# Optimization experiments

Measured on AMD Instinct MI355X. Metric: run time of the kernel, lower is better.

The kernel has to match this reference:

```python
import jax, jax.numpy as jnp
import numpy as np

L, H, C, D = 4, 4, 64, 64  # layers, heads, per-head out channels, embedding_dim
NEG_SLOPE = 0.2
LN_EPS = 1e-5

def layer_norm(x, g, b):
    mu = x.mean(-1, keepdims=True)
    var = ((x - mu) ** 2).mean(-1, keepdims=True)
    return (x - mu) * jax.lax.rsqrt(var + LN_EPS) * g + b

def setup_inputs() -> dict:
    key = jax.random.key(0)
    N, E = 20000, 320000
    ks = jax.random.split(key, 12)
    f = lambda k, shape: jax.random.normal(k, shape, jnp.float32) * 0.1
    return {
        "node_feats": jax.random.normal(ks[0], (N, D), jnp.float32),
        "edge_feats": jax.random.normal(ks[1], (E, D), jnp.float32),
        "edge_index": jax.random.randint(ks[2], (2, E), 0, N),
        "W_lin": f(ks[3], (L, D, H * C)),      # GAT node projection (bias=False)
        "W_edge": f(ks[4], (L, D, H * C)),     # GAT edge projection (bias=False)
        "att_src": f(ks[5], (L, H, C)),
        "att_dst": f(ks[6], (L, H, C)),
        "att_edge": f(ks[7], (L, H, C)),
        "bias_conv": f(ks[8], (L, D)),
        "ln_g": jnp.ones((L, D), jnp.float32),
        "ln_b": jnp.zeros((L, D), jnp.float32),
        "eW1": f(ks[9], (L, 3 * D, 3 * D)),
        "eb1": jnp.zeros((L, 3 * D), jnp.float32),
        "eln_g": jnp.ones((L, 3 * D), jnp.float32),
        "eln_b": jnp.zeros((L, 3 * D), jnp.float32),
        "eW2": f(ks[10], (L, 3 * D, D)),
        "eb2": jnp.zeros((L, D), jnp.float32),
    }

def reference(node_feats, edge_feats, edge_index, W_lin, W_edge, att_src,
              att_dst, att_edge, bias_conv, ln_g, ln_b, eW1, eb1, eln_g,
              eln_b, eW2, eb2):
    N = node_feats.shape[0]
    src, dst = edge_index[0], edge_index[1]
    for l in range(L):
        # --- GAT attention conv (concat=False: mean over heads) ---
        x = (node_feats @ W_lin[l]).reshape(N, H, C)
        e = (edge_feats @ W_edge[l]).reshape(-1, H, C)
        x_j, x_i = x[src], x[dst]                                  # [E,H,C]
        alpha = ((x_j * att_src[l]).sum(-1) + (x_i * att_dst[l]).sum(-1)
                 + (e * att_edge[l]).sum(-1))                      # [E,H]
        alpha = jax.nn.leaky_relu(alpha, NEG_SLOPE)
        amax = jax.ops.segment_max(alpha, dst, num_segments=N)
        alpha = jnp.exp(alpha - amax[dst])
        denom = jax.ops.segment_sum(alpha, dst, num_segments=N)
        alpha = alpha / (denom[dst] + 1e-16)
        out = jax.ops.segment_sum(x_j * alpha[..., None], dst, num_segments=N)
        out = out.mean(axis=1) + bias_conv[l]                      # [N,D]
        node_feats = layer_norm(out, ln_g[l], ln_b[l])
        # --- SparseEdgeUpdateLayer (residual=True) ---
        ni, nj = node_feats[src], node_feats[dst]
        h = jnp.concatenate([ni + nj, jnp.abs(ni - nj), edge_feats], axis=-1)
        h = jax.nn.relu(layer_norm(h @ eW1[l] + eb1[l], eln_g[l], eln_b[l]))
        edge_feats = h @ eW2[l] + eb2[l] + edge_feats
        # dropout is identity in eval mode
        if l < L - 1:
            node_feats = jax.nn.relu(node_feats)
    return node_feats, edge_feats
```

## Files before the change

kernel.cpp:

```cpp
#include <hip/hip_runtime.h>
#include <math.h>

#define NLAYERS 4
#define H 4
#define C 64
#define D 64
#define HC 256
#define D3 192
#define NEG 0.2f

typedef float f32x4 __attribute__((ext_vector_type(4)));
typedef short bf16x8 __attribute__((ext_vector_type(8)));
typedef unsigned short u16;

__device__ __forceinline__ u16 f2bf(float f) {
    unsigned u = __float_as_uint(f);
    u += 0x7FFFu + ((u >> 16) & 1u);
    return (u16)(u >> 16);
}
__device__ __forceinline__ float bf2f(u16 h) {
    return __uint_as_float((unsigned)h << 16);
}

__global__ void k_weffs(const float* __restrict__ W_edge, const float* __restrict__ att_edge,
                        const float* __restrict__ W_lin, const float* __restrict__ att_s,
                        const float* __restrict__ att_d,
                        float* __restrict__ weff, float* __restrict__ w_asd) {
    int l = blockIdx.x;
    const float* We = W_edge + (size_t)l * D * HC;
    const float* Wl = W_lin + (size_t)l * D * HC;
    const float* ae = att_edge + l * H * C;
    const float* as_ = att_s + l * H * C;
    const float* ad = att_d + l * H * C;
    int t = threadIdx.x;
    int d = t >> 2, h = t & 3;
    float se = 0.f, ss = 0.f, sd = 0.f;
    #pragma unroll
    for (int c = 0; c < C; ++c) {
        float we = We[d * HC + h * C + c];
        float wl = Wl[d * HC + h * C + c];
        se = fmaf(we, ae[h * C + c], se);
        ss = fmaf(wl, as_[h * C + c], ss);
        sd = fmaf(wl, ad[h * C + c], sd);
    }
    weff[l * HC + d * 4 + h] = se;
    w_asd[l * 512 + d * 8 + h] = ss;
    w_asd[l * 512 + d * 8 + 4 + h] = sd;
}

__global__ void k_cvtw(const float* __restrict__ W1, const float* __restrict__ W2,
                       u16* __restrict__ W1T, u16* __restrict__ W2T) {
    int i = blockIdx.x * 256 + threadIdx.x;
    if (i < NLAYERS * D3 * D3) {
        int l = i / (D3 * D3), r = i % (D3 * D3);
        int n = r / D3, k = r % D3;
        W1T[i] = f2bf(W1[l * D3 * D3 + k * D3 + n]);
    } else {
        int j = i - NLAYERS * D3 * D3;
        if (j < NLAYERS * D3 * D) {
            int l = j / (D3 * D), r = j % (D3 * D);
            int n = r / D3, k = r % D3;
            W2T[j] = f2bf(W2[l * D3 * D + k * D + n]);
        }
    }
}

__global__ void k_cvtwl(const float* __restrict__ W_lin,
                        u16* __restrict__ WTh, u16* __restrict__ WTl) {
    int i = blockIdx.x * 256 + threadIdx.x;
    if (i >= NLAYERS * HC * D) return;
    int l = i / (HC * D), r = i % (HC * D);
    int o = r / D, d = r % D;
    float v = W_lin[(size_t)l * D * HC + d * HC + o];
    u16 h = f2bf(v);
    WTh[i] = h;
    WTl[i] = f2bf(v - bf2f(h));
}

__global__ void k_hist(const int* __restrict__ dst, int* __restrict__ deg, int E) {
    int i = blockIdx.x * blockDim.x + threadIdx.x;
    if (i < E) atomicAdd(&deg[dst[i]], 1);
}

__global__ void k_scan(const int* __restrict__ deg, int* __restrict__ rowptr,
                       int* __restrict__ head, int N, int E) {
    __shared__ int lds[1024];
    int t = threadIdx.x;
    int chunk = (N + 1023) / 1024;
    int begin = t * chunk, end = min(begin + chunk, N);
    int sum = 0;
    for (int i = begin; i < end; ++i) sum += deg[i];
    lds[t] = sum;
    __syncthreads();
    for (int off = 1; off < 1024; off <<= 1) {
        int v = (t >= off) ? lds[t - off] : 0;
        __syncthreads();
        lds[t] += v;
        __syncthreads();
    }
    int running = (t == 0) ? 0 : lds[t - 1];
    for (int i = begin; i < end; ++i) {
        int dg = deg[i];
        rowptr[i] = running;
        head[i] = running;
        running += dg;
    }
    if (t == 0) rowptr[N] = E;
}

__global__ void k_scatter(const int* __restrict__ src, const int* __restrict__ dst,
                          int* __restrict__ head, int* __restrict__ csrpos,
                          int* __restrict__ perm_src, int E) {
    int i = blockIdx.x * blockDim.x + threadIdx.x;
    if (i < E) {
        int d = dst[i];
        int pos = atomicAdd(&head[d], 1);
        csrpos[i] = pos;
        perm_src[pos] = src[i];
    }
}

__global__ __launch_bounds__(256, 4) void k_nodeproj_mfma(
    const float* __restrict__ nf, const u16* __restrict__ WTh, const u16* __restrict__ WTl,
    const float* __restrict__ w_asd, float* __restrict__ x,
    float* __restrict__ a_src, float* __restrict__ a_dst, int N, int relu_in) {
    __shared__ __align__(16) u16 s_ah[32 * 72];
    __shared__ __align__(16) u16 s_al[32 * 72];
    __shared__ __align__(16) float s_nf[32][68];
    __shared__ __align__(16) float s_wasd[512];
    int tid = threadIdx.x;
    int w = tid >> 6, lane = tid & 63;
    int n0 = blockIdx.x << 5;

    if (tid < 128) *(float4*)&s_wasd[tid * 4] = *(const float4*)&w_asd[tid * 4];

    {
        int r = tid >> 3, c0 = (tid & 7) << 3;
        int n = n0 + r;
        float4 v0 = make_float4(0.f, 0.f, 0.f, 0.f), v1 = v0;
        if (n < N) {
            v0 = *(const float4*)&nf[(size_t)n * D + c0];
            v1 = *(const float4*)&nf[(size_t)n * D + c0 + 4];
        }
        if (relu_in) {
            v0.x = fmaxf(v0.x, 0.f); v0.y = fmaxf(v0.y, 0.f);
            v0.z = fmaxf(v0.z, 0.f); v0.w = fmaxf(v0.w, 0.f);
            v1.x = fmaxf(v1.x, 0.f); v1.y = fmaxf(v1.y, 0.f);
            v1.z = fmaxf(v1.z, 0.f); v1.w = fmaxf(v1.w, 0.f);
        }
        *(float4*)&s_nf[r][c0] = v0;
        *(float4*)&s_nf[r][c0 + 4] = v1;
        float vv[8] = {v0.x, v0.y, v0.z, v0.w, v1.x, v1.y, v1.z, v1.w};
        bf16x8 hv, lv;
        #pragma unroll
        for (int j = 0; j < 8; ++j) {
            u16 h = f2bf(vv[j]);
            hv[j] = (short)h;
            lv[j] = (short)f2bf(vv[j] - bf2f(h));
        }
        *(bf16x8*)&s_ah[r * 72 + c0] = hv;
        *(bf16x8*)&s_al[r * 72 + c0] = lv;
    }
    __syncthreads();

    int m16 = lane & 15, quad = lane >> 4, kq = quad * 8;
    f32x4 acc[2][4];
    #pragma unroll
    for (int mt = 0; mt < 2; ++mt)
        #pragma unroll
        for (int nt = 0; nt < 4; ++nt) {
            acc[mt][nt][0] = 0.f; acc[mt][nt][1] = 0.f;
            acc[mt][nt][2] = 0.f; acc[mt][nt][3] = 0.f;
        }
    #pragma unroll
    for (int ks = 0; ks < 2; ++ks) {
        int ko = ks * 32 + kq;
        bf16x8 ah0 = *(const bf16x8*)&s_ah[m16 * 72 + ko];
        bf16x8 ah1 = *(const bf16x8*)&s_ah[(16 + m16) * 72 + ko];
        bf16x8 al0 = *(const bf16x8*)&s_al[m16 * 72 + ko];
        bf16x8 al1 = *(const bf16x8*)&s_al[(16 + m16) * 72 + ko];
        #pragma unroll
        for (int nt = 0; nt < 4; ++nt) {
            int col = w * 64 + nt * 16 + m16;
            bf16x8 bh = *(const bf16x8*)&WTh[col * D + ko];
            bf16x8 bl = *(const bf16x8*)&WTl[col * D + ko];
            acc[0][nt] = __builtin_amdgcn_mfma_f32_16x16x32_bf16(ah0, bh, acc[0][nt], 0, 0, 0);
            acc[0][nt] = __builtin_amdgcn_mfma_f32_16x16x32_bf16(al0, bh, acc[0][nt], 0, 0, 0);
            acc[0][nt] = __builtin_amdgcn_mfma_f32_16x16x32_bf16(ah0, bl, acc[0][nt], 0, 0, 0);
            acc[1][nt] = __builtin_amdgcn_mfma_f32_16x16x32_bf16(ah1, bh, acc[1][nt], 0, 0, 0);
            acc[1][nt] = __builtin_amdgcn_mfma_f32_16x16x32_bf16(al1, bh, acc[1][nt], 0, 0, 0);
            acc[1][nt] = __builtin_amdgcn_mfma_f32_16x16x32_bf16(ah1, bl, acc[1][nt], 0, 0, 0);
        }
    }
    #pragma unroll
    for (int mt = 0; mt < 2; ++mt) {
        #pragma unroll
        for (int nt = 0; nt < 4; ++nt) {
            int col = w * 64 + nt * 16 + m16;
            #pragma unroll
            for (int r = 0; r < 4; ++r) {
                int n = n0 + mt * 16 + quad * 4 + r;
                if (n < N) x[(size_t)n * HC + col] = acc[mt][nt][r];
            }
        }
    }

    {
        int nloc = tid >> 3, o = tid & 7;
        float s = 0.f;
        #pragma unroll
        for (int d = 0; d < 64; ++d)
            s = fmaf(s_nf[nloc][d], s_wasd[d * 8 + o], s);
        int n = n0 + nloc;
        if (n < N) {
            if (o < 4) a_src[n * 4 + o] = s;
            else       a_dst[n * 4 + (o - 4)] = s;
        }
    }
}

__global__ void k_alpha(const float* __restrict__ ef, const float* __restrict__ weff,
                        const int* __restrict__ src, const int* __restrict__ dst,
                        const float* __restrict__ a_src, const float* __restrict__ a_dst,
                        const int* __restrict__ csrpos, float* __restrict__ alpha_csr, int E) {
    int wave = (int)((blockIdx.x * blockDim.x + threadIdx.x) >> 6);
    int lane = threadIdx.x & 63;
    int sub = lane >> 4, li = lane & 15;
    int e = wave * 4 + sub;
    if (e >= E) return;
    float4 efv = *(const float4*)&ef[(size_t)e * D + li * 4];
    float4 w0 = *(const float4*)&weff[(li * 4 + 0) * 4];
    float4 w1 = *(const float4*)&weff[(li * 4 + 1) * 4];
    float4 w2 = *(const float4*)&weff[(li * 4 + 2) * 4];
    float4 w3 = *(const float4*)&weff[(li * 4 + 3) * 4];
    float p0 = efv.x * w0.x + efv.y * w1.x + efv.z * w2.x + efv.w * w3.x;
    float p1 = efv.x * w0.y + efv.y * w1.y + efv.z * w2.y + efv.w * w3.y;
    float p2 = efv.x * w0.z + efv.y * w1.z + efv.z * w2.z + efv.w * w3.z;
    float p3 = efv.x * w0.w + efv.y * w1.w + efv.z * w2.w + efv.w * w3.w;
    #pragma unroll
    for (int off = 1; off < 16; off <<= 1) {
        p0 += __shfl_xor(p0, off);
        p1 += __shfl_xor(p1, off);
        p2 += __shfl_xor(p2, off);
        p3 += __shfl_xor(p3, off);
    }
    if (li < 4) {
        float p = (li == 0) ? p0 : (li == 1) ? p1 : (li == 2) ? p2 : p3;
        int s = src[e], dd = dst[e];
        float a = p + a_src[s * 4 + li] + a_dst[dd * 4 + li];
        a = (a > 0.f) ? a : NEG * a;
        alpha_csr[(size_t)csrpos[e] * 4 + li] = a;
    }
}

__global__ void k_alpha_lite(const float* __restrict__ palpha,
                             const int* __restrict__ src, const int* __restrict__ dst,
                             const float* __restrict__ a_src, const float* __restrict__ a_dst,
                             const int* __restrict__ csrpos, float* __restrict__ alpha_csr, int E) {
    int i = blockIdx.x * 256 + threadIdx.x;
    if (i >= E * 4) return;
    int e = i >> 2, h = i & 3;
    float a = palpha[i] + a_src[src[e] * 4 + h] + a_dst[dst[e] * 4 + h];
    a = (a > 0.f) ? a : NEG * a;
    alpha_csr[(size_t)csrpos[e] * 4 + h] = a;
}

__global__ void k_gat(const float* __restrict__ x, float* __restrict__ alpha_csr,
                      const int* __restrict__ rowptr, const int* __restrict__ perm_src,
                      const float* __restrict__ bias, const float* __restrict__ g,
                      const float* __restrict__ b, float* __restrict__ nf_ln,
                      float* __restrict__ out2, int N) {
    int n = (int)((blockIdx.x * blockDim.x + threadIdx.x) >> 6);
    int lane = threadIdx.x & 63;
    if (n >= N) return;
    int s = rowptr[n], e = rowptr[n + 1];
    int deg = e - s;
    float m0 = -1e30f, m1 = -1e30f, m2 = -1e30f, m3 = -1e30f;
    for (int i = lane; i < deg; i += 64) {
        const float4 a = *(const float4*)&alpha_csr[(size_t)(s + i) * 4];
        m0 = fmaxf(m0, a.x); m1 = fmaxf(m1, a.y);
        m2 = fmaxf(m2, a.z); m3 = fmaxf(m3, a.w);
    }
    #pragma unroll
    for (int off = 32; off; off >>= 1) {
        m0 = fmaxf(m0, __shfl_xor(m0, off)); m1 = fmaxf(m1, __shfl_xor(m1, off));
        m2 = fmaxf(m2, __shfl_xor(m2, off)); m3 = fmaxf(m3, __shfl_xor(m3, off));
    }
    float d0 = 0.f, d1 = 0.f, d2 = 0.f, d3 = 0.f;
    for (int i = lane; i < deg; i += 64) {
        float4 a = *(const float4*)&alpha_csr[(size_t)(s + i) * 4];
        a.x = expf(a.x - m0); a.y = expf(a.y - m1);
        a.z = expf(a.z - m2); a.w = expf(a.w - m3);
        *(float4*)&alpha_csr[(size_t)(s + i) * 4] = a;
        d0 += a.x; d1 += a.y; d2 += a.z; d3 += a.w;
    }
    #pragma unroll
    for (int off = 32; off; off >>= 1) {
        d0 += __shfl_xor(d0, off); d1 += __shfl_xor(d1, off);
        d2 += __shfl_xor(d2, off); d3 += __shfl_xor(d3, off);
    }
    float i0 = 0.25f / (d0 + 1e-16f), i1 = 0.25f / (d1 + 1e-16f);
    float i2 = 0.25f / (d2 + 1e-16f), i3 = 0.25f / (d3 + 1e-16f);
    float ac0 = 0.f, ac1 = 0.f, ac2 = 0.f, ac3 = 0.f;
    int j = 0;
    for (; j + 3 < deg; j += 4) {
        const float4 a0 = *(const float4*)&alpha_csr[(size_t)(s + j + 0) * 4];
        const float4 a1 = *(const float4*)&alpha_csr[(size_t)(s + j + 1) * 4];
        const float4 a2 = *(const float4*)&alpha_csr[(size_t)(s + j + 2) * 4];
        const float4 a3 = *(const float4*)&alpha_csr[(size_t)(s + j + 3) * 4];
        int s0 = perm_src[s + j + 0], s1 = perm_src[s + j + 1];
        int s2 = perm_src[s + j + 2], s3 = perm_src[s + j + 3];
        const float* x0 = x + (size_t)s0 * HC;
        const float* x1 = x + (size_t)s1 * HC;
        const float* x2 = x + (size_t)s2 * HC;
        const float* x3 = x + (size_t)s3 * HC;
        ac0 += a0.x * i0 * x0[lane] + a0.y * i1 * x0[64 + lane]
             + a0.z * i2 * x0[128 + lane] + a0.w * i3 * x0[192 + lane];
        ac1 += a1.x * i0 * x1[lane] + a1.y * i1 * x1[64 + lane]
             + a1.z * i2 * x1[128 + lane] + a1.w * i3 * x1[192 + lane];
        ac2 += a2.x * i0 * x2[lane] + a2.y * i1 * x2[64 + lane]
             + a2.z * i2 * x2[128 + lane] + a2.w * i3 * x2[192 + lane];
        ac3 += a3.x * i0 * x3[lane] + a3.y * i1 * x3[64 + lane]
             + a3.z * i2 * x3[128 + lane] + a3.w * i3 * x3[192 + lane];
    }
    for (; j < deg; ++j) {
        const float4 a = *(const float4*)&alpha_csr[(size_t)(s + j) * 4];
        int sidx = perm_src[s + j];
        const float* xr = x + (size_t)sidx * HC;
        ac0 += a.x * i0 * xr[lane] + a.y * i1 * xr[64 + lane]
             + a.z * i2 * xr[128 + lane] + a.w * i3 * xr[192 + lane];
    }
    float acc = (ac0 + ac1) + (ac2 + ac3);
    float v = acc + bias[lane];
    float sm = v;
    #pragma unroll
    for (int off = 32; off; off >>= 1) sm += __shfl_xor(sm, off);
    float mu = sm * (1.f / 64.f);
    float dv = v - mu;
    float q = dv * dv;
    #pragma unroll
    for (int off = 32; off; off >>= 1) q += __shfl_xor(q, off);
    float rstd = rsqrtf(q * (1.f / 64.f) + 1e-5f);
    float r = dv * rstd * g[lane] + b[lane];
    nf_ln[(size_t)n * D + lane] = r;
    if (out2) out2[(size_t)n * D + lane] = r;
}

__global__ __launch_bounds__(256, 5) void k_edgemlp_mfma(
    const float* __restrict__ nf, const float* __restrict__ ef_in,
    const int* __restrict__ src, const int* __restrict__ dst,
    const u16* __restrict__ W1T, const float* __restrict__ b1,
    const float* __restrict__ lg, const float* __restrict__ lb,
    const u16* __restrict__ W2T, const float* __restrict__ b2,
    float* __restrict__ ef_out, const float* __restrict__ weffN,
    float* __restrict__ palpha, int E) {
    __shared__ __align__(16) u16 A1[64 * 200];
    __shared__ float ps[4][64], pq[4][64];
    int tid = threadIdx.x;
    int w = tid >> 6, lane = tid & 63;
    int e0 = blockIdx.x * 64;
    int ebase = e0 + w * 16;

    int idxv = 0;
    if (lane < 16)      idxv = src[min(ebase + lane, E - 1)];
    else if (lane < 32) idxv = dst[min(ebase + lane - 16, E - 1)];

    {
        int half = lane >> 5;
        int c2 = (lane & 31) << 1;
        #pragma unroll
        for (int it = 0; it < 8; ++it) {
            int eloc = 2 * it + half;
            int ge = ebase + eloc;
            int sA = __shfl(idxv, eloc);
            int dA = __shfl(idxv, 16 + eloc);
            float2 za = make_float2(0.f, 0.f), zb = za, zf = za;
            if (ge < E) {
                za = *(const float2*)&nf[(size_t)sA * D + c2];
                zb = *(const float2*)&nf[(size_t)dA * D + c2];
                zf = *(const float2*)&ef_in[(size_t)ge * D + c2];
            }
            unsigned su = (unsigned)f2bf(za.x + zb.x) | ((unsigned)f2bf(za.y + zb.y) << 16);
            unsigned du = (unsigned)f2bf(fabsf(za.x - zb.x)) | ((unsigned)f2bf(fabsf(za.y - zb.y)) << 16);
            unsigned fu = (unsigned)f2bf(zf.x) | ((unsigned)f2bf(zf.y) << 16);
            int row = w * 16 + eloc;
            *(unsigned*)&A1[row * 200 + c2]       = su;
            *(unsigned*)&A1[row * 200 + 64 + c2]  = du;
            *(unsigned*)&A1[row * 200 + 128 + c2] = fu;
        }
    }
    __syncthreads();

    int m16 = lane & 15, quad = lane >> 4, kq = quad * 8;
    f32x4 acc[4][3];
    #pragma unroll
    for (int nt = 0; nt < 3; ++nt) {
        float bv = b1[w * 48 + nt * 16 + m16];
        #pragma unroll
        for (int mt = 0; mt < 4; ++mt) {
            acc[mt][nt][0] = bv; acc[mt][nt][1] = bv;
            acc[mt][nt][2] = bv; acc[mt][nt][3] = bv;
        }
    }
    #pragma unroll
    for (int ks = 0; ks < 6; ++ks) {
        int ko = ks * 32 + kq;
        bf16x8 af0 = *(const bf16x8*)&A1[(0  + m16) * 200 + ko];
        bf16x8 af1 = *(const bf16x8*)&A1[(16 + m16) * 200 + ko];
        bf16x8 af2 = *(const bf16x8*)&A1[(32 + m16) * 200 + ko];
        bf16x8 af3 = *(const bf16x8*)&A1[(48 + m16) * 200 + ko];
        #pragma unroll
        for (int nt = 0; nt < 3; ++nt) {
            bf16x8 bfr = *(const bf16x8*)&W1T[(w * 48 + nt * 16 + m16) * D3 + ko];
            acc[0][nt] = __builtin_amdgcn_mfma_f32_16x16x32_bf16(af0, bfr, acc[0][nt], 0, 0, 0);
            acc[1][nt] = __builtin_amdgcn_mfma_f32_16x16x32_bf16(af1, bfr, acc[1][nt], 0, 0, 0);
            acc[2][nt] = __builtin_amdgcn_mfma_f32_16x16x32_bf16(af2, bfr, acc[2][nt], 0, 0, 0);
            acc[3][nt] = __builtin_amdgcn_mfma_f32_16x16x32_bf16(af3, bfr, acc[3][nt], 0, 0, 0);
        }
    }

    #pragma unroll
    for (int mt = 0; mt < 4; ++mt) {
        float s8[4], q8[4];
        #pragma unroll
        for (int r = 0; r < 4; ++r) {
            float v0 = acc[mt][0][r], v1 = acc[mt][1][r], v2 = acc[mt][2][r];
            s8[r] = v0 + v1 + v2;
            q8[r] = v0 * v0 + v1 * v1 + v2 * v2;
        }
        #pragma unroll
        for (int off = 1; off < 16; off <<= 1) {
            #pragma unroll
            for (int r = 0; r < 4; ++r) {
                s8[r] += __shfl_xor(s8[r], off);
                q8[r] += __shfl_xor(q8[r], off);
            }
        }
        if (m16 == 0) {
            #pragma unroll
            for (int r = 0; r < 4; ++r) {
                int row = mt * 16 + quad * 4 + r;
                ps[w][row] = s8[r];
                pq[w][row] = q8[r];
            }
        }
    }
    __syncthreads();

    float mu_l, rs_l;
    {
        float s = ps[0][lane] + ps[1][lane] + ps[2][lane] + ps[3][lane];
        float q = pq[0][lane] + pq[1][lane] + pq[2][lane] + pq[3][lane];
        mu_l = s * (1.f / 192.f);
        rs_l = rsqrtf(q * (1.f / 192.f) - mu_l * mu_l + 1e-5f);
    }

    {
        float gg0 = lg[w * 48 + 0 * 16 + m16], bb0 = lb[w * 48 + 0 * 16 + m16];
        float gg1 = lg[w * 48 + 1 * 16 + m16], bb1 = lb[w * 48 + 1 * 16 + m16];
        float gg2 = lg[w * 48 + 2 * 16 + m16], bb2 = lb[w * 48 + 2 * 16 + m16];
        #pragma unroll
        for (int mt = 0; mt < 4; ++mt) {
            #pragma unroll
            for (int r = 0; r < 4; ++r) {
                int row = mt * 16 + quad * 4 + r;
                float mu = __shfl(mu_l, row);
                float rstd = __shfl(rs_l, row);
                float v0 = (acc[mt][0][r] - mu) * rstd * gg0 + bb0;
                float v1 = (acc[mt][1][r] - mu) * rstd * gg1 + bb1;
                float v2 = (acc[mt][2][r] - mu) * rstd * gg2 + bb2;
                A1[row * 200 + w * 48 + 0 * 16 + m16] = f2bf(fmaxf(v0, 0.f));
                A1[row * 200 + w * 48 + 1 * 16 + m16] = f2bf(fmaxf(v1, 0.f));
                A1[row * 200 + w * 48 + 2 * 16 + m16] = f2bf(fmaxf(v2, 0.f));
            }
        }
    }
    __syncthreads();

    int col2 = w * 16 + m16;
    f32x4 acc2[4];
    {
        float bv = b2[col2];
        #pragma unroll
        for (int mt = 0; mt < 4; ++mt) {
            acc2[mt][0] = bv; acc2[mt][1] = bv; acc2[mt][2] = bv; acc2[mt][3] = bv;
        }
    }
    #pragma unroll
    for (int ks = 0; ks < 6; ++ks) {
        int ko = ks * 32 + kq;
        bf16x8 b2f = *(const bf16x8*)&W2T[col2 * D3 + ko];
        bf16x8 a2f0 = *(const bf16x8*)&A1[(0  + m16) * 200 + ko];
        bf16x8 a2f1 = *(const bf16x8*)&A1[(16 + m16) * 200 + ko];
        bf16x8 a2f2 = *(const bf16x8*)&A1[(32 + m16) * 200 + ko];
        bf16x8 a2f3 = *(const bf16x8*)&A1[(48 + m16) * 200 + ko];
        acc2[0] = __builtin_amdgcn_mfma_f32_16x16x32_bf16(a2f0, b2f, acc2[0], 0, 0, 0);
        acc2[1] = __builtin_amdgcn_mfma_f32_16x16x32_bf16(a2f1, b2f, acc2[1], 0, 0, 0);
        acc2[2] = __builtin_amdgcn_mfma_f32_16x16x32_bf16(a2f2, b2f, acc2[2], 0, 0, 0);
        acc2[3] = __builtin_amdgcn_mfma_f32_16x16x32_bf16(a2f3, b2f, acc2[3], 0, 0, 0);
    }
    #pragma unroll
    for (int mt = 0; mt < 4; ++mt) {
        int row0 = mt * 16 + quad * 4;
        #pragma unroll
        for (int r = 0; r < 4; ++r) {
            int ge = e0 + row0 + r;
            float v = 0.f;
            if (ge < E) {
                size_t o = (size_t)ge * D + col2;
                v = acc2[mt][r] + ef_in[o];
                ef_out[o] = v;
            }
            acc2[mt][r] = v;
        }
    }

    if (palpha) {
        __syncthreads();
        float* A1f = (float*)A1;
        #pragma unroll
        for (int mt = 0; mt < 4; ++mt) {
            #pragma unroll
            for (int r = 0; r < 4; ++r)
                A1f[(mt * 16 + quad * 4 + r) * 68 + col2] = acc2[mt][r];
        }
        float* wst = &ps[0][0];
        if (tid < 64) *(float4*)&wst[tid * 4] = *(const float4*)&weffN[tid * 4];
        __syncthreads();
        int e = tid >> 2, h = tid & 3;
        int ge = e0 + e;
        float p = 0.f;
        #pragma unroll
        for (int d = 0; d < 64; ++d)
            p = fmaf(A1f[e * 68 + d], wst[d * 4 + h], p);
        if (ge < E) palpha[(size_t)ge * 4 + h] = p;
    }
}

extern "C" void kernel_launch(void* const* d_in, const int* in_sizes, int n_in,
                              void* d_out, int out_size, void* d_ws, size_t ws_size,
                              hipStream_t stream) {
    const float* nf_in0   = (const float*)d_in[0];
    const float* ef_in0   = (const float*)d_in[1];
    const int*   eidx     = (const int*)d_in[2];
    const float* W_lin    = (const float*)d_in[3];
    const float* W_edge   = (const float*)d_in[4];
    const float* att_src  = (const float*)d_in[5];
    const float* att_dst  = (const float*)d_in[6];
    const float* att_edge = (const float*)d_in[7];
    const float* biasc    = (const float*)d_in[8];
    const float* ln_g     = (const float*)d_in[9];
    const float* ln_b     = (const float*)d_in[10];
    const float* eW1      = (const float*)d_in[11];
    const float* eb1      = (const float*)d_in[12];
    const float* eln_g    = (const float*)d_in[13];
    const float* eln_b    = (const float*)d_in[14];
    const float* eW2      = (const float*)d_in[15];
    const float* eb2      = (const float*)d_in[16];

    int N = in_sizes[0] / D;
    int E = in_sizes[1] / D;
    const int* srcp = eidx;
    const int* dstp = eidx + E;

    float* ws        = (float*)d_ws;
    float* x         = ws;
    float* alpha_csr = x + (size_t)N * HC;
    float* a_src     = alpha_csr + (size_t)E * H;
    float* a_dst     = a_src + (size_t)N * H;
    float* nf_ln     = a_dst + (size_t)N * H;
    float* weff      = nf_ln + (size_t)N * D;
    float* w_asd     = weff + NLAYERS * HC;
    u16*   W1T       = (u16*)(w_asd + NLAYERS * 512);
    u16*   W2T       = W1T + (size_t)NLAYERS * D3 * D3;
    u16*   WLh       = W2T + (size_t)NLAYERS * D3 * D;
    u16*   WLl       = WLh + (size_t)NLAYERS * HC * D;
    int*   rowptr    = (int*)(WLl + (size_t)NLAYERS * HC * D);
    int*   head      = rowptr + (N + 1);
    int*   csrpos    = head + N;
    int*   perm_src  = csrpos + (size_t)E;
    float* palpha    = (float*)(perm_src + (size_t)E);

    float* out_nf = (float*)d_out;
    float* out_ef = out_nf + (size_t)N * D;

    {
        int total = NLAYERS * D3 * D3 + NLAYERS * D3 * D;
        k_cvtw<<<(total + 255) / 256, 256, 0, stream>>>(eW1, eW2, W1T, W2T);
        k_cvtwl<<<(NLAYERS * HC * D + 255) / 256, 256, 0, stream>>>(W_lin, WLh, WLl);
        k_weffs<<<NLAYERS, 256, 0, stream>>>(W_edge, att_edge, W_lin, att_src, att_dst,
                                             weff, w_asd);
        hipMemsetAsync(head, 0, (size_t)N * sizeof(int), stream);
        k_hist<<<(E + 255) / 256, 256, 0, stream>>>(dstp, head, E);
        k_scan<<<1, 1024, 0, stream>>>(head, rowptr, head, N, E);
        k_scatter<<<(E + 255) / 256, 256, 0, stream>>>(srcp, dstp, head, csrpos, perm_src, E);
    }

    for (int l = 0; l < NLAYERS; ++l) {
        const float* nf_cur = (l == 0) ? nf_in0 : nf_ln;
        const float* ef_cur = (l == 0) ? ef_in0 : out_ef;
        int relu_in = (l > 0) ? 1 : 0;

        k_nodeproj_mfma<<<(N + 31) / 32, 256, 0, stream>>>(
            nf_cur, WLh + (size_t)l * HC * D, WLl + (size_t)l * HC * D,
            w_asd + (size_t)l * 512, x, a_src, a_dst, N, relu_in);
        if (l == 0) {
            k_alpha<<<(E + 15) / 16, 256, 0, stream>>>(ef_cur, weff + (size_t)l * HC,
                                                       srcp, dstp, a_src, a_dst,
                                                       csrpos, alpha_csr, E);
        } else {
            k_alpha_lite<<<(E * 4 + 255) / 256, 256, 0, stream>>>(palpha, srcp, dstp,
                                                                  a_src, a_dst,
                                                                  csrpos, alpha_csr, E);
        }
        k_gat<<<(N + 3) / 4, 256, 0, stream>>>(x, alpha_csr, rowptr, perm_src,
                                               biasc + l * D, ln_g + l * D, ln_b + l * D,
                                               nf_ln, (l == NLAYERS - 1) ? out_nf : nullptr, N);
        const float* weffN = (l < NLAYERS - 1) ? (weff + (size_t)(l + 1) * HC) : nullptr;
        float* pout = (l < NLAYERS - 1) ? palpha : nullptr;
        k_edgemlp_mfma<<<(E + 63) / 64, 256, 0, stream>>>(nf_ln, ef_cur, srcp, dstp,
                                                          W1T + (size_t)l * D3 * D3, eb1 + l * D3,
                                                          eln_g + l * D3, eln_b + l * D3,
                                                          W2T + (size_t)l * D3 * D, eb2 + l * D,
                                                          out_ef, weffN, pout, E);
    }
}
```

Baseline: 1.007 ms.

## Make each wave own full edge rows in edge MLP, removing block barriers

The edge-MLP kernel is restructured so each wave computes all 192 hidden columns for its own 16 edges. The LayerNorm statistics can then be reduced with intra-wave shuffles, so the shared-memory partial-sum exchange and every __syncthreads are removed. The attention-weight staging is done per wave, and the launch-bounds occupancy hint drops from 5 to 4. In exchange, each wave now loads the whole W1T and W2T weight set from global memory instead of a quarter of it, which raises cache traffic.

```diff
diff --git a/kernel.cpp b/kernel.cpp
--- a/kernel.cpp
+++ b/kernel.cpp
@@ -346,7 +346,7 @@
     if (out2) out2[(size_t)n * D + lane] = r;
 }
 
-__global__ __launch_bounds__(256, 5) void k_edgemlp_mfma(
+__global__ __launch_bounds__(256, 4) void k_edgemlp_mfma(
     const float* __restrict__ nf, const float* __restrict__ ef_in,
     const int* __restrict__ src, const int* __restrict__ dst,
     const u16* __restrict__ W1T, const float* __restrict__ b1,
@@ -355,11 +355,14 @@
     float* __restrict__ ef_out, const float* __restrict__ weffN,
     float* __restrict__ palpha, int E) {
     __shared__ __align__(16) u16 A1[64 * 200];
-    __shared__ float ps[4][64], pq[4][64];
+    __shared__ float wstg[256];
     int tid = threadIdx.x;
     int w = tid >> 6, lane = tid & 63;
     int e0 = blockIdx.x * 64;
     int ebase = e0 + w * 16;
+    int m16 = lane & 15, quad = lane >> 4, kq = quad * 8;
+
+    if (weffN) *(float4*)&wstg[lane * 4] = *(const float4*)&weffN[lane * 4];
 
     int idxv = 0;
     if (lane < 16)      idxv = src[min(ebase + lane, E - 1)];
@@ -389,150 +392,103 @@
             *(unsigned*)&A1[row * 200 + 128 + c2] = fu;
         }
     }
-    __syncthreads();
-
-    int m16 = lane & 15, quad = lane >> 4, kq = quad * 8;
-    f32x4 acc[4][3];
-    #pragma unroll
-    for (int nt = 0; nt < 3; ++nt) {
-        float bv = b1[w * 48 + nt * 16 + m16];
-        #pragma unroll
-        for (int mt = 0; mt < 4; ++mt) {
-            acc[mt][nt][0] = bv; acc[mt][nt][1] = bv;
-            acc[mt][nt][2] = bv; acc[mt][nt][3] = bv;
-        }
+
+    f32x4 acc[12];
+    #pragma unroll
+    for (int nt = 0; nt < 12; ++nt) {
+        float bv = b1[nt * 16 + m16];
+        acc[nt][0] = bv; acc[nt][1] = bv; acc[nt][2] = bv; acc[nt][3] = bv;
     }
     #pragma unroll
     for (int ks = 0; ks < 6; ++ks) {
         int ko = ks * 32 + kq;
-        bf16x8 af0 = *(const bf16x8*)&A1[(0  + m16) * 200 + ko];
-        bf16x8 af1 = *(const bf16x8*)&A1[(16 + m16) * 200 + ko];
-        bf16x8 af2 = *(const bf16x8*)&A1[(32 + m16) * 200 + ko];
-        bf16x8 af3 = *(const bf16x8*)&A1[(48 + m16) * 200 + ko];
-        #pragma unroll
-        for (int nt = 0; nt < 3; ++nt) {
-            bf16x8 bfr = *(const bf16x8*)&W1T[(w * 48 + nt * 16 + m16) * D3 + ko];
-            acc[0][nt] = __builtin_amdgcn_mfma_f32_16x16x32_bf16(af0, bfr, acc[0][nt], 0, 0, 0);
-            acc[1][nt] = __builtin_amdgcn_mfma_f32_16x16x32_bf16(af1, bfr, acc[1][nt], 0, 0, 0);
-            acc[2][nt] = __builtin_amdgcn_mfma_f32_16x16x32_bf16(af2, bfr, acc[2][nt], 0, 0, 0);
-            acc[3][nt] = __builtin_amdgcn_mfma_f32_16x16x32_bf16(af3, bfr, acc[3][nt], 0, 0, 0);
-        }
-    }
-
-    #pragma unroll
-    for (int mt = 0; mt < 4; ++mt) {
-        float s8[4], q8[4];
+        bf16x8 af = *(const bf16x8*)&A1[(w * 16 + m16) * 200 + ko];
+        #pragma unroll
+        for (int nt = 0; nt < 12; ++nt) {
+            bf16x8 bfr = *(const bf16x8*)&W1T[(nt * 16 + m16) * D3 + ko];
+            acc[nt] = __builtin_amdgcn_mfma_f32_16x16x32_bf16(af, bfr, acc[nt], 0, 0, 0);
+        }
+    }
+
+    float s4[4], q4[4];
+    #pragma unroll
+    for (int r = 0; r < 4; ++r) {
+        float s = 0.f, q = 0.f;
+        #pragma unroll
+        for (int nt = 0; nt < 12; ++nt) { float v = acc[nt][r]; s += v; q += v * v; }
+        s4[r] = s; q4[r] = q;
+    }
+    #pragma unroll
+    for (int off = 1; off < 16; off <<= 1) {
         #pragma unroll
         for (int r = 0; r < 4; ++r) {
-            float v0 = acc[mt][0][r], v1 = acc[mt][1][r], v2 = acc[mt][2][r];
-            s8[r] = v0 + v1 + v2;
-            q8[r] = v0 * v0 + v1 * v1 + v2 * v2;
-        }
-        #pragma unroll
-        for (int off = 1; off < 16; off <<= 1) {
-            #pragma unroll
-            for (int r = 0; r < 4; ++r) {
-                s8[r] += __shfl_xor(s8[r], off);
-                q8[r] += __shfl_xor(q8[r], off);
-            }
-        }
-        if (m16 == 0) {
-            #pragma unroll
-            for (int r = 0; r < 4; ++r) {
-                int row = mt * 16 + quad * 4 + r;
-                ps[w][row] = s8[r];
-                pq[w][row] = q8[r];
-            }
-        }
-    }
-    __syncthreads();
-
-    float mu_l, rs_l;
-    {
-        float s = ps[0][lane] + ps[1][lane] + ps[2][lane] + ps[3][lane];
-        float q = pq[0][lane] + pq[1][lane] + pq[2][lane] + pq[3][lane];
-        mu_l = s * (1.f / 192.f);
-        rs_l = rsqrtf(q * (1.f / 192.f) - mu_l * mu_l + 1e-5f);
-    }
-
-    {
-        float gg0 = lg[w * 48 + 0 * 16 + m16], bb0 = lb[w * 48 + 0 * 16 + m16];
-        float gg1 = lg[w * 48 + 1 * 16 + m16], bb1 = lb[w * 48 + 1 * 16 + m16];
-        float gg2 = lg[w * 48 + 2 * 16 + m16], bb2 = lb[w * 48 + 2 * 16 + m16];
-        #pragma unroll
-        for (int mt = 0; mt < 4; ++mt) {
-            #pragma unroll
-            for (int r = 0; r < 4; ++r) {
-                int row = mt * 16 + quad * 4 + r;
-                float mu = __shfl(mu_l, row);
-                float rstd = __shfl(rs_l, row);
-                float v0 = (acc[mt][0][r] - mu) * rstd * gg0 + bb0;
-                float v1 = (acc[mt][1][r] - mu) * rstd * gg1 + bb1;
-                float v2 = (acc[mt][2][r] - mu) * rstd * gg2 + bb2;
-                A1[row * 200 + w * 48 + 0 * 16 + m16] = f2bf(fmaxf(v0, 0.f));
-                A1[row * 200 + w * 48 + 1 * 16 + m16] = f2bf(fmaxf(v1, 0.f));
-                A1[row * 200 + w * 48 + 2 * 16 + m16] = f2bf(fmaxf(v2, 0.f));
-            }
-        }
-    }
-    __syncthreads();
-
-    int col2 = w * 16 + m16;
+            s4[r] += __shfl_xor(s4[r], off);
+            q4[r] += __shfl_xor(q4[r], off);
+        }
+    }
+    float mu[4], rs[4];
+    #pragma unroll
+    for (int r = 0; r < 4; ++r) {
+        mu[r] = s4[r] * (1.f / 192.f);
+        rs[r] = rsqrtf(q4[r] * (1.f / 192.f) - mu[r] * mu[r] + 1e-5f);
+    }
+
+    #pragma unroll
+    for (int nt = 0; nt < 12; ++nt) {
+        float gg = lg[nt * 16 + m16], bb = lb[nt * 16 + m16];
+        #pragma unroll
+        for (int r = 0; r < 4; ++r) {
+            int row = w * 16 + quad * 4 + r;
+            float v = (acc[nt][r] - mu[r]) * rs[r] * gg + bb;
+            A1[row * 200 + nt * 16 + m16] = f2bf(fmaxf(v, 0.f));
+        }
+    }
+
     f32x4 acc2[4];
-    {
-        float bv = b2[col2];
-        #pragma unroll
-        for (int mt = 0; mt < 4; ++mt) {
-            acc2[mt][0] = bv; acc2[mt][1] = bv; acc2[mt][2] = bv; acc2[mt][3] = bv;
-        }
+    #pragma unroll
+    for (int nt = 0; nt < 4; ++nt) {
+        float bv = b2[nt * 16 + m16];
+        acc2[nt][0] = bv; acc2[nt][1] = bv; acc2[nt][2] = bv; acc2[nt][3] = bv;
     }
     #pragma unroll
     for (int ks = 0; ks < 6; ++ks) {
         int ko = ks * 32 + kq;
-        bf16x8 b2f = *(const bf16x8*)&W2T[col2 * D3 + ko];
-        bf16x8 a2f0 = *(const bf16x8*)&A1[(0  + m16) * 200 + ko];
-        bf16x8 a2f1 = *(const bf16x8*)&A1[(16 + m16) * 200 + ko];
-        bf16x8 a2f2 = *(const bf16x8*)&A1[(32 + m16) * 200 + ko];
-        bf16x8 a2f3 = *(const bf16x8*)&A1[(48 + m16) * 200 + ko];
-        acc2[0] = __builtin_amdgcn_mfma_f32_16x16x32_bf16(a2f0, b2f, acc2[0], 0, 0, 0);
-        acc2[1] = __builtin_amdgcn_mfma_f32_16x16x32_bf16(a2f1, b2f, acc2[1], 0, 0, 0);
-        acc2[2] = __builtin_amdgcn_mfma_f32_16x16x32_bf16(a2f2, b2f, acc2[2], 0, 0, 0);
-        acc2[3] = __builtin_amdgcn_mfma_f32_16x16x32_bf16(a2f3, b2f, acc2[3], 0, 0, 0);
-    }
-    #pragma unroll
-    for (int mt = 0; mt < 4; ++mt) {
-        int row0 = mt * 16 + quad * 4;
+        bf16x8 a2 = *(const bf16x8*)&A1[(w * 16 + m16) * 200 + ko];
+        #pragma unroll
+        for (int nt = 0; nt < 4; ++nt) {
+            bf16x8 b2f = *(const bf16x8*)&W2T[(nt * 16 + m16) * D3 + ko];
+            acc2[nt] = __builtin_amdgcn_mfma_f32_16x16x32_bf16(a2, b2f, acc2[nt], 0, 0, 0);
+        }
+    }
+
+    #pragma unroll
+    for (int nt = 0; nt < 4; ++nt) {
         #pragma unroll
         for (int r = 0; r < 4; ++r) {
-            int ge = e0 + row0 + r;
+            int ge = ebase + quad * 4 + r;
             float v = 0.f;
             if (ge < E) {
-                size_t o = (size_t)ge * D + col2;
-                v = acc2[mt][r] + ef_in[o];
+                size_t o = (size_t)ge * D + nt * 16 + m16;
+                v = acc2[nt][r] + ef_in[o];
                 ef_out[o] = v;
             }
-            acc2[mt][r] = v;
+            acc2[nt][r] = v;
         }
     }
 
     if (palpha) {
-        __syncthreads();
-        float* A1f = (float*)A1;
-        #pragma unroll
-        for (int mt = 0; mt < 4; ++mt) {
+        float* A1fw = (float*)&A1[w * 16 * 200];
+        #pragma unroll
+        for (int nt = 0; nt < 4; ++nt)
             #pragma unroll
             for (int r = 0; r < 4; ++r)
-                A1f[(mt * 16 + quad * 4 + r) * 68 + col2] = acc2[mt][r];
-        }
-        float* wst = &ps[0][0];
-        if (tid < 64) *(float4*)&wst[tid * 4] = *(const float4*)&weffN[tid * 4];
-        __syncthreads();
-        int e = tid >> 2, h = tid & 3;
-        int ge = e0 + e;
+                A1fw[(quad * 4 + r) * 68 + nt * 16 + m16] = acc2[nt][r];
+        int e = lane >> 2, h = lane & 3;
+        int ge = ebase + e;
         float p = 0.f;
         #pragma unroll
         for (int d = 0; d < 64; ++d)
-            p = fmaf(A1f[e * 68 + d], wst[d * 4 + h], p);
+            p = fmaf(A1fw[e * 68 + d], wstg[d * 4 + h], p);
         if (ge < E) palpha[(size_t)ge * 4 + h] = p;
     }
 }
```

Result: slower. 1.554 ms (+54.3%).
